# Optimization experiments

Measured on AMD Instinct MI355X. Metric: run time of the kernel, lower is better.

## Reference

```python
import jax, jax.numpy as jnp
import numpy as np

RADIUS = 0.5
NEG_INF = -jnp.inf


def setup_inputs() -> dict:
    key = jax.random.key(0)
    ks = jax.random.split(key, 10)
    N_q, N_o, pos_dim, latent_dim = 2048, 2048, 3, 64
    enc_dim = 3 * pos_dim  # q_pos, o_pos, rel
    inp = {
        "h_obs": jax.random.normal(ks[0], (N_o, latent_dim), dtype=jnp.float32),
        "x_obs": jax.random.normal(ks[1], (N_o, latent_dim), dtype=jnp.float32),
        "pos_obs": jax.random.uniform(ks[2], (N_o, pos_dim), dtype=jnp.float32),
        "pos_query": jax.random.uniform(ks[3], (N_q, pos_dim), dtype=jnp.float32),
        # kernel_mlp: Linear(enc_dim->latent) + ReLU + Linear(latent->1)
        "W1": jax.random.normal(ks[4], (enc_dim, latent_dim), dtype=jnp.float32) / np.sqrt(enc_dim),
        "b1": jnp.zeros((latent_dim,), dtype=jnp.float32),
        "W2": jax.random.normal(ks[5], (latent_dim, 1), dtype=jnp.float32) / np.sqrt(latent_dim),
        "b2": jnp.zeros((1,), dtype=jnp.float32),
        # value_proj: Linear(latent->latent)
        "Wv": jax.random.normal(ks[6], (latent_dim, latent_dim), dtype=jnp.float32) / np.sqrt(latent_dim),
        "bv": jnp.zeros((latent_dim,), dtype=jnp.float32),
    }
    return inp


def reference(h_obs, x_obs, pos_obs, pos_query, W1, b1, W2, b2, Wv, bv):
    # rel: [N_q, N_o, pos_dim]
    rel = pos_query[:, None, :] - pos_obs[None, :, :]
    N_q, N_o, _ = rel.shape
    pos_q_exp = jnp.broadcast_to(pos_query[:, None, :], rel.shape)
    pos_o_exp = jnp.broadcast_to(pos_obs[None, :, :], rel.shape)
    kernel_input = jnp.concatenate([pos_q_exp, pos_o_exp, rel], axis=-1)  # [N_q, N_o, 3*pos_dim]
    # small pointwise MLP over all pairs
    hidden = jax.nn.relu(jnp.einsum('qoe,el->qol', kernel_input, W1) + b1)  # [N_q, N_o, latent]
    logits = jnp.einsum('qol,lk->qok', hidden, W2)[..., 0] + b2[0]          # [N_q, N_o]
    # radius mask
    dist = jnp.linalg.norm(rel, axis=-1)
    logits = jnp.where(dist > RADIUS, NEG_INF, logits)
    # softmax over observations (dim=1)
    weights = jax.nn.softmax(logits, axis=1)  # [N_q, N_o]
    v = h_obs @ Wv + bv                        # [N_o, latent]
    h_query = weights @ v                      # [N_q, latent]
    return h_query
```

## Files before the change

kernel.cpp:

```cpp
#include <hip/hip_runtime.h>

#define NQ 2048
#define NO 2048
#define NOC 32

constexpr size_t OFF_PH = 0;
constexpr size_t OFF_PS = (size_t)NOC * NQ * 64;

__global__ __launch_bounds__(256, 6) void gano_main(
    const float* __restrict__ h_obs,
    const float* __restrict__ pos_obs,
    const float* __restrict__ pos_query,
    const float* __restrict__ W1,
    const float* __restrict__ b1,
    const float* __restrict__ W2,
    float* __restrict__ Ph,
    float* __restrict__ Ps)
{
    __shared__ __align__(16) float wtab[64 * 8];
    __shared__ __align__(16) float tl[64 * 32];
    __shared__ float po[3 * 32];
    __shared__ float ue[32 * 64];
    __shared__ float sbuf[4 * 64];

    const int tid  = threadIdx.x;
    const int lane = tid & 63;
    const int wave = __builtin_amdgcn_readfirstlane(tid >> 6);
    const int qg = blockIdx.x >> 5;
    const int oc = blockIdx.x & 31;
    const int q  = qg * 64 + lane;
    const int ow = wave * 8;
    const int lw = wave * 16;

    if (tid < 64) {
        float w0 = W1[0*64+tid], w1_ = W1[1*64+tid], w2_ = W1[2*64+tid];
        float w3 = W1[3*64+tid], w4  = W1[4*64+tid], w5  = W1[5*64+tid];
        float w6 = W1[6*64+tid], w7  = W1[7*64+tid], w8  = W1[8*64+tid];
        float* r = wtab + tid * 8;
        r[0] = w0 + w6;  r[1] = w1_ + w7;  r[2] = w2_ + w8;
        r[3] = b1[tid];  r[4] = W2[tid];
        r[5] = w3 - w6;  r[6] = w4 - w7;   r[7] = w5 - w8;
    }
    float pq0 = pos_query[q * 3 + 0];
    float pq1 = pos_query[q * 3 + 1];
    float pq2 = pos_query[q * 3 + 2];
    __syncthreads();

    float h0 = 0.f, h1 = 0.f, h2 = 0.f, h3 = 0.f, h4 = 0.f, h5 = 0.f, h6 = 0.f, h7 = 0.f;
    float h8 = 0.f, h9 = 0.f, hA = 0.f, hB = 0.f, hC = 0.f, hD = 0.f, hE = 0.f, hF = 0.f;
    float spart = 0.f;

#pragma unroll
    for (int st = 0; st < 2; ++st) {
        const int ob = oc * 64 + st * 32;

        {
            const int o = lane & 31, half = lane >> 5;
            float p0 = pos_obs[(ob + o) * 3 + 0];
            float p1 = pos_obs[(ob + o) * 3 + 1];
            float p2 = pos_obs[(ob + o) * 3 + 2];
            if (wave == 0 && half == 0) { po[o] = p0; po[32 + o] = p1; po[64 + o] = p2; }
#pragma unroll
            for (int j = 0; j < 8; ++j) {
                int l = wave * 16 + j * 2 + half;
                const float* r = wtab + l * 8;
                tl[l * 32 + o] = p0 * r[5] + p1 * r[6] + p2 * r[7];
            }
        }
        __syncthreads();

        float lg[8];
#pragma unroll
        for (int o = 0; o < 8; ++o) lg[o] = 0.f;
#pragma unroll 16
        for (int l = 0; l < 64; ++l) {
            float4 c4 = *(const float4*)(wtab + l * 8);
            float wl  = wtab[l * 8 + 4];
            float u   = fmaf(pq2, c4.z, fmaf(pq1, c4.y, fmaf(pq0, c4.x, c4.w)));
            float4 ta = *(const float4*)(tl + l * 32 + ow);
            float4 tb = *(const float4*)(tl + l * 32 + ow + 4);
            lg[0] += wl * fmaxf(u + ta.x, 0.f);
            lg[1] += wl * fmaxf(u + ta.y, 0.f);
            lg[2] += wl * fmaxf(u + ta.z, 0.f);
            lg[3] += wl * fmaxf(u + ta.w, 0.f);
            lg[4] += wl * fmaxf(u + tb.x, 0.f);
            lg[5] += wl * fmaxf(u + tb.y, 0.f);
            lg[6] += wl * fmaxf(u + tb.z, 0.f);
            lg[7] += wl * fmaxf(u + tb.w, 0.f);
        }
#pragma unroll
        for (int o = 0; o < 8; ++o) {
            float d0 = pq0 - po[ow + o];
            float d1 = pq1 - po[32 + ow + o];
            float d2 = pq2 - po[64 + ow + o];
            float dd = d0 * d0 + d1 * d1 + d2 * d2;
            float ev = (dd > 0.25f) ? 0.f : __expf(lg[o]);
            spart += ev;
            ue[(ow + o) * 64 + lane] = ev;
        }
        __syncthreads();

#pragma unroll 4
        for (int o = 0; o < 32; ++o) {
            float eo = ue[o * 64 + lane];
            const float4* hr = (const float4*)(h_obs + (size_t)(ob + o) * 64 + lw);
            float4 v0 = hr[0], v1 = hr[1], v2 = hr[2], v3 = hr[3];
            h0 += eo * v0.x; h1 += eo * v0.y; h2 += eo * v0.z; h3 += eo * v0.w;
            h4 += eo * v1.x; h5 += eo * v1.y; h6 += eo * v1.z; h7 += eo * v1.w;
            h8 += eo * v2.x; h9 += eo * v2.y; hA += eo * v2.z; hB += eo * v2.w;
            hC += eo * v3.x; hD += eo * v3.y; hE += eo * v3.z; hF += eo * v3.w;
        }
    }

    float* hp = Ph + ((size_t)oc * NQ + (size_t)qg * 64 + lane) * 64 + lw;
    ((float4*)hp)[0] = make_float4(h0, h1, h2, h3);
    ((float4*)hp)[1] = make_float4(h4, h5, h6, h7);
    ((float4*)hp)[2] = make_float4(h8, h9, hA, hB);
    ((float4*)hp)[3] = make_float4(hC, hD, hE, hF);
    sbuf[wave * 64 + lane] = spart;
    __syncthreads();
    if (wave == 0) {
        float s = sbuf[lane] + sbuf[64 + lane] + sbuf[128 + lane] + sbuf[192 + lane];
        Ps[(size_t)oc * NQ + (size_t)qg * 64 + lane] = s;
    }
}

__global__ __launch_bounds__(256, 2) void gano_comb(
    const float* __restrict__ Ph,
    const float* __restrict__ Ps,
    const float* __restrict__ Wv,
    const float* __restrict__ bv,
    float* __restrict__ out)
{
    __shared__ __align__(16) float wv[64 * 64];
    __shared__ __align__(16) float g[4 * 68];
    const int tid  = threadIdx.x;
    const int lane = tid & 63;
    const int wave = tid >> 6;
    const int q0 = blockIdx.x * 4;
    {
        const float4* src = (const float4*)Wv;
        float4* dst = (float4*)wv;
#pragma unroll
        for (int k = 0; k < 4; ++k) dst[tid + k * 256] = src[tid + k * 256];
    }
    {
        const int qi = wave, k = lane;
        float acc = 0.f;
#pragma unroll
        for (int c = 0; c < NOC; ++c)
            acc += Ph[((size_t)c * NQ + q0 + qi) * 64 + k];
        g[qi * 68 + k] = acc;
        if (k == 0) {
            float ss = 0.f;
#pragma unroll
            for (int c = 0; c < NOC; ++c) ss += Ps[(size_t)c * NQ + q0 + qi];
            g[qi * 68 + 64] = ss;
        }
    }
    __syncthreads();
    const float* gq = g + wave * 68;
    float inv = 1.0f / gq[64];
    float a0 = 0.f, a1 = 0.f, a2 = 0.f, a3 = 0.f;
#pragma unroll
    for (int kb = 0; kb < 16; ++kb) {
        float4 g4 = *(const float4*)(gq + kb * 4);
        a0 += g4.x * wv[(kb * 4 + 0) * 64 + lane];
        a1 += g4.y * wv[(kb * 4 + 1) * 64 + lane];
        a2 += g4.z * wv[(kb * 4 + 2) * 64 + lane];
        a3 += g4.w * wv[(kb * 4 + 3) * 64 + lane];
    }
    out[(size_t)(q0 + wave) * 64 + lane] = ((a0 + a1) + (a2 + a3)) * inv + bv[lane];
}

extern "C" void kernel_launch(void* const* d_in, const int* in_sizes, int n_in,
                              void* d_out, int out_size, void* d_ws, size_t ws_size,
                              hipStream_t stream) {
    const float* h_obs     = (const float*)d_in[0];
    const float* pos_obs   = (const float*)d_in[2];
    const float* pos_query = (const float*)d_in[3];
    const float* W1        = (const float*)d_in[4];
    const float* b1        = (const float*)d_in[5];
    const float* W2        = (const float*)d_in[6];
    const float* Wv        = (const float*)d_in[8];
    const float* bv        = (const float*)d_in[9];
    float* ws  = (float*)d_ws;
    float* out = (float*)d_out;

    gano_main<<<dim3(1024), dim3(256), 0, stream>>>(h_obs, pos_obs, pos_query,
                                                    W1, b1, W2, ws + OFF_PH, ws + OFF_PS);
    gano_comb<<<dim3(NQ / 4), dim3(256), 0, stream>>>(ws + OFF_PH, ws + OFF_PS, Wv, bv, out);
}
```

Baseline: 116.3 us.

## Compute obs-position term per pair in registers and drop two-stage obs loop

Each wave now loads its 16 observation positions as wave-uniform scalars and computes the per-hidden-unit observation contribution with three FMAs per pair, instead of precomputing it into a shared-memory table. The two 32-observation stages are merged into a single 64-observation pass, which removes several barriers and the tl/po shared tables. The trade is about two extra FMAs per pair-hidden element and more registers (16 logits plus 48 position values), which may lower occupancy under the 6-block launch bound.

```diff
diff --git a/kernel.cpp b/kernel.cpp
--- a/kernel.cpp
+++ b/kernel.cpp
@@ -6,6 +6,11 @@
 
 constexpr size_t OFF_PH = 0;
 constexpr size_t OFF_PS = (size_t)NOC * NQ * 64;
+
+__device__ __forceinline__ float rfl(float x) {
+    int i = __builtin_amdgcn_readfirstlane(__builtin_bit_cast(int, x));
+    return __builtin_bit_cast(float, i);
+}
 
 __global__ __launch_bounds__(256, 6) void gano_main(
     const float* __restrict__ h_obs,
@@ -17,10 +22,8 @@
     float* __restrict__ Ph,
     float* __restrict__ Ps)
 {
-    __shared__ __align__(16) float wtab[64 * 8];
-    __shared__ __align__(16) float tl[64 * 32];
-    __shared__ float po[3 * 32];
-    __shared__ float ue[32 * 64];
+    __shared__ __align__(16) float cf[64 * 8];
+    __shared__ float ue[64 * 64];
     __shared__ float sbuf[4 * 64];
 
     const int tid  = threadIdx.x;
@@ -28,15 +31,15 @@
     const int wave = __builtin_amdgcn_readfirstlane(tid >> 6);
     const int qg = blockIdx.x >> 5;
     const int oc = blockIdx.x & 31;
+    const int obase = oc * 64;
     const int q  = qg * 64 + lane;
-    const int ow = wave * 8;
-    const int lw = wave * 16;
+    const int ow = wave * 16;
 
     if (tid < 64) {
         float w0 = W1[0*64+tid], w1_ = W1[1*64+tid], w2_ = W1[2*64+tid];
         float w3 = W1[3*64+tid], w4  = W1[4*64+tid], w5  = W1[5*64+tid];
         float w6 = W1[6*64+tid], w7  = W1[7*64+tid], w8  = W1[8*64+tid];
-        float* r = wtab + tid * 8;
+        float* r = cf + tid * 8;
         r[0] = w0 + w6;  r[1] = w1_ + w7;  r[2] = w2_ + w8;
         r[3] = b1[tid];  r[4] = W2[tid];
         r[5] = w3 - w6;  r[6] = w4 - w7;   r[7] = w5 - w8;
@@ -44,81 +47,68 @@
     float pq0 = pos_query[q * 3 + 0];
     float pq1 = pos_query[q * 3 + 1];
     float pq2 = pos_query[q * 3 + 2];
+
+    float px[16], py[16], pz[16];
+    {
+        const float* pob = pos_obs + __builtin_amdgcn_readfirstlane((obase + ow) * 3);
+#pragma unroll
+        for (int o = 0; o < 16; ++o) {
+            px[o] = rfl(pob[o * 3 + 0]);
+            py[o] = rfl(pob[o * 3 + 1]);
+            pz[o] = rfl(pob[o * 3 + 2]);
+        }
+    }
+    __syncthreads();
+
+    float lg[16];
+#pragma unroll
+    for (int o = 0; o < 16; ++o) lg[o] = 0.f;
+#pragma unroll 4
+    for (int l = 0; l < 64; ++l) {
+        float4 ca = *(const float4*)(cf + l * 8);
+        float4 cb = *(const float4*)(cf + l * 8 + 4);
+        float u = fmaf(pq2, ca.z, fmaf(pq1, ca.y, fmaf(pq0, ca.x, ca.w)));
+#pragma unroll
+        for (int o = 0; o < 16; ++o) {
+            float acc = fmaf(cb.y, px[o], u);
+            acc = fmaf(cb.z, py[o], acc);
+            acc = fmaf(cb.w, pz[o], acc);
+            lg[o] = fmaf(cb.x, fmaxf(acc, 0.f), lg[o]);
+        }
+    }
+
+    float spart = 0.f;
+#pragma unroll
+    for (int o = 0; o < 16; ++o) {
+        float d0 = pq0 - px[o];
+        float d1 = pq1 - py[o];
+        float d2 = pq2 - pz[o];
+        float dd = d0 * d0 + d1 * d1 + d2 * d2;
+        float ev = (dd > 0.25f) ? 0.f : __expf(lg[o]);
+        spart += ev;
+        ue[(ow + o) * 64 + lane] = ev;
+    }
+    sbuf[wave * 64 + lane] = spart;
     __syncthreads();
 
     float h0 = 0.f, h1 = 0.f, h2 = 0.f, h3 = 0.f, h4 = 0.f, h5 = 0.f, h6 = 0.f, h7 = 0.f;
     float h8 = 0.f, h9 = 0.f, hA = 0.f, hB = 0.f, hC = 0.f, hD = 0.f, hE = 0.f, hF = 0.f;
-    float spart = 0.f;
-
-#pragma unroll
-    for (int st = 0; st < 2; ++st) {
-        const int ob = oc * 64 + st * 32;
-
-        {
-            const int o = lane & 31, half = lane >> 5;
-            float p0 = pos_obs[(ob + o) * 3 + 0];
-            float p1 = pos_obs[(ob + o) * 3 + 1];
-            float p2 = pos_obs[(ob + o) * 3 + 2];
-            if (wave == 0 && half == 0) { po[o] = p0; po[32 + o] = p1; po[64 + o] = p2; }
-#pragma unroll
-            for (int j = 0; j < 8; ++j) {
-                int l = wave * 16 + j * 2 + half;
-                const float* r = wtab + l * 8;
-                tl[l * 32 + o] = p0 * r[5] + p1 * r[6] + p2 * r[7];
-            }
-        }
-        __syncthreads();
-
-        float lg[8];
-#pragma unroll
-        for (int o = 0; o < 8; ++o) lg[o] = 0.f;
-#pragma unroll 16
-        for (int l = 0; l < 64; ++l) {
-            float4 c4 = *(const float4*)(wtab + l * 8);
-            float wl  = wtab[l * 8 + 4];
-            float u   = fmaf(pq2, c4.z, fmaf(pq1, c4.y, fmaf(pq0, c4.x, c4.w)));
-            float4 ta = *(const float4*)(tl + l * 32 + ow);
-            float4 tb = *(const float4*)(tl + l * 32 + ow + 4);
-            lg[0] += wl * fmaxf(u + ta.x, 0.f);
-            lg[1] += wl * fmaxf(u + ta.y, 0.f);
-            lg[2] += wl * fmaxf(u + ta.z, 0.f);
-            lg[3] += wl * fmaxf(u + ta.w, 0.f);
-            lg[4] += wl * fmaxf(u + tb.x, 0.f);
-            lg[5] += wl * fmaxf(u + tb.y, 0.f);
-            lg[6] += wl * fmaxf(u + tb.z, 0.f);
-            lg[7] += wl * fmaxf(u + tb.w, 0.f);
-        }
-#pragma unroll
-        for (int o = 0; o < 8; ++o) {
-            float d0 = pq0 - po[ow + o];
-            float d1 = pq1 - po[32 + ow + o];
-            float d2 = pq2 - po[64 + ow + o];
-            float dd = d0 * d0 + d1 * d1 + d2 * d2;
-            float ev = (dd > 0.25f) ? 0.f : __expf(lg[o]);
-            spart += ev;
-            ue[(ow + o) * 64 + lane] = ev;
-        }
-        __syncthreads();
-
 #pragma unroll 4
-        for (int o = 0; o < 32; ++o) {
-            float eo = ue[o * 64 + lane];
-            const float4* hr = (const float4*)(h_obs + (size_t)(ob + o) * 64 + lw);
-            float4 v0 = hr[0], v1 = hr[1], v2 = hr[2], v3 = hr[3];
-            h0 += eo * v0.x; h1 += eo * v0.y; h2 += eo * v0.z; h3 += eo * v0.w;
-            h4 += eo * v1.x; h5 += eo * v1.y; h6 += eo * v1.z; h7 += eo * v1.w;
-            h8 += eo * v2.x; h9 += eo * v2.y; hA += eo * v2.z; hB += eo * v2.w;
-            hC += eo * v3.x; hD += eo * v3.y; hE += eo * v3.z; hF += eo * v3.w;
-        }
+    for (int o = 0; o < 64; ++o) {
+        float eo = ue[o * 64 + lane];
+        const float4* hr = (const float4*)(h_obs + (size_t)(obase + o) * 64 + ow);
+        float4 v0 = hr[0], v1 = hr[1], v2 = hr[2], v3 = hr[3];
+        h0 += eo * v0.x; h1 += eo * v0.y; h2 += eo * v0.z; h3 += eo * v0.w;
+        h4 += eo * v1.x; h5 += eo * v1.y; h6 += eo * v1.z; h7 += eo * v1.w;
+        h8 += eo * v2.x; h9 += eo * v2.y; hA += eo * v2.z; hB += eo * v2.w;
+        hC += eo * v3.x; hD += eo * v3.y; hE += eo * v3.z; hF += eo * v3.w;
     }
 
-    float* hp = Ph + ((size_t)oc * NQ + (size_t)qg * 64 + lane) * 64 + lw;
+    float* hp = Ph + ((size_t)oc * NQ + (size_t)qg * 64 + lane) * 64 + ow;
     ((float4*)hp)[0] = make_float4(h0, h1, h2, h3);
     ((float4*)hp)[1] = make_float4(h4, h5, h6, h7);
     ((float4*)hp)[2] = make_float4(h8, h9, hA, hB);
     ((float4*)hp)[3] = make_float4(hC, hD, hE, hF);
-    sbuf[wave * 64 + lane] = spart;
-    __syncthreads();
     if (wave == 0) {
         float s = sbuf[lane] + sbuf[64 + lane] + sbuf[128 + lane] + sbuf[192 + lane];
         Ps[(size_t)oc * NQ + (size_t)qg * 64 + lane] = s;
```

Measured after the change: 120.7 us. 3.8% more time.
